# Performance work log

Measured on AMD Instinct MI355X. Metric: run time of the kernel, lower is better.

## Reference

```python
import jax, jax.numpy as jnp
import numpy as np

MODEL_DIM = 1024
ATTEN_DIM = 64
HEAD_NUM = 16
EPS = 1e-5


def setup_inputs() -> dict:
    key = jax.random.key(0)
    ks = jax.random.split(key, 10)
    B, S, D = 4, 2048, MODEL_DIM
    H = ATTEN_DIM * HEAD_NUM
    s = 1.0 / np.sqrt(D)
    return {
        "Q": jax.random.normal(ks[0], (B, S, D), dtype=jnp.float32),
        "Wq": jax.random.normal(ks[1], (D, H), dtype=jnp.float32) * s,
        "bq": jnp.zeros((H,), dtype=jnp.float32),
        "Wk": jax.random.normal(ks[2], (D, H), dtype=jnp.float32) * s,
        "bk": jnp.zeros((H,), dtype=jnp.float32),
        "Wv": jax.random.normal(ks[3], (D, H), dtype=jnp.float32) * s,
        "bv": jnp.zeros((H,), dtype=jnp.float32),
        "Wo": jax.random.normal(ks[4], (H, D), dtype=jnp.float32) * s,
        "bo": jnp.zeros((D,), dtype=jnp.float32),
        "ln_g": jnp.ones((D,), dtype=jnp.float32),
        "ln_b": jnp.zeros((D,), dtype=jnp.float32),
    }


def _layernorm(x, g, b):
    mu = jnp.mean(x, axis=-1, keepdims=True)
    var = jnp.var(x, axis=-1, keepdims=True)
    return (x - mu) * jax.lax.rsqrt(var + EPS) * g + b


def reference(Q, Wq, bq, Wk, bk, Wv, bv, Wo, bo, ln_g, ln_b):
    B, S, D = Q.shape
    residual = Q
    # projections -> [B, H, S, d]
    q = (Q @ Wq + bq).reshape(B, S, HEAD_NUM, ATTEN_DIM).transpose(0, 2, 1, 3)
    k = (Q @ Wk + bk).reshape(B, S, HEAD_NUM, ATTEN_DIM).transpose(0, 2, 1, 3)
    v = (Q @ Wv + bv).reshape(B, S, HEAD_NUM, ATTEN_DIM).transpose(0, 2, 1, 3)
    scores = jnp.einsum("bhqd,bhkd->bhqk", q, k) / np.sqrt(ATTEN_DIM).astype(np.float32)
    attn = jax.nn.softmax(scores, axis=-1)
    context = jnp.einsum("bhqk,bhkd->bhqd", attn, v)
    context = context.transpose(0, 2, 1, 3).reshape(B, S, HEAD_NUM * ATTEN_DIM)
    output = context @ Wo + bo  # dropout p=0.0 -> identity
    return _layernorm(output + residual, ln_g, ln_b)
```

## Files before the change

### kernel.cpp

```cpp
#include <hip/hip_runtime.h>
#include <math.h>

#define BATCH 4
#define SEQ 2048
#define DMODEL 1024
#define NHEAD 16
#define DHEAD 64
#define MTOT (BATCH * SEQ)
#define LN_EPS 1e-5f

typedef float f4 __attribute__((ext_vector_type(4)));
typedef float f32x4 __attribute__((ext_vector_type(4)));
typedef __bf16 bf16_t;
typedef __bf16 bf16x8 __attribute__((ext_vector_type(8)));
typedef __bf16 bf16x4 __attribute__((ext_vector_type(4)));

__device__ __forceinline__ void gload_lds16(const bf16_t* g, bf16_t* l) {
    __builtin_amdgcn_global_load_lds(
        (const __attribute__((address_space(1))) void*)g,
        (__attribute__((address_space(3))) void*)l, 16, 0, 0);
}

__global__ __launch_bounds__(256) void cvt_bf16(
    const float* __restrict__ x, bf16_t* __restrict__ y, int n4)
{
    for (int i = blockIdx.x * 256 + threadIdx.x; i < n4; i += gridDim.x * 256) {
        f4 v = *(const f4*)&x[(size_t)i * 4];
        bf16x4 o;
        o[0] = (bf16_t)v[0]; o[1] = (bf16_t)v[1];
        o[2] = (bf16_t)v[2]; o[3] = (bf16_t)v[3];
        *(bf16x4*)&y[(size_t)i * 4] = o;
    }
}

__global__ __launch_bounds__(256) void wtrans4(
    const float* __restrict__ W0, const float* __restrict__ W1,
    const float* __restrict__ W2, const float* __restrict__ W3,
    bf16_t* __restrict__ Wt)
{
    __shared__ float tile[32][33];
    const int z = blockIdx.z;
    const float* W = (z == 0) ? W0 : (z == 1) ? W1 : (z == 2) ? W2 : W3;
    bf16_t* dst = Wt + (size_t)z * DMODEL * DMODEL;
    const int n0 = blockIdx.x * 32, k0 = blockIdx.y * 32;
    const int c = threadIdx.x & 31, rr = threadIdx.x >> 5;
#pragma unroll
    for (int i = 0; i < 32; i += 8)
        tile[rr + i][c] = W[(size_t)(k0 + rr + i) * DMODEL + n0 + c];
    __syncthreads();
#pragma unroll
    for (int i = 0; i < 32; i += 8)
        dst[(size_t)(n0 + rr + i) * DMODEL + k0 + c] = (bf16_t)tile[c][rr + i];
}

template<int OUT_BF16, int FUSED3>
__global__ __launch_bounds__(256) void gemm_mfma(
    const bf16_t* __restrict__ A, const bf16_t* __restrict__ Bt,
    const float* __restrict__ bias0, const float* __restrict__ bias1,
    const float* __restrict__ bias2, void* __restrict__ Cout)
{
    __shared__ bf16_t As[2][4096];
    __shared__ bf16_t Bs[2][4096];
    const int t = threadIdx.x;
    const int w = t >> 6, lane = t & 63;
    const int r16 = lane & 15, g = lane >> 4;

    const int flat = blockIdx.x;
    const int xc = flat & 7;
    const int t2 = flat >> 3;
    int nx, my;
    if (FUSED3) { nx = t2 % 24; my = 8 * xc + t2 / 24; }
    else        { nx = t2 & 7;  my = 8 * xc + (t2 >> 3); }
    const int m0 = my * 128, n0 = nx * 128;
    const int wr = w >> 1, wc = w & 1;

    const int y0 = w * 1024 + lane * 16;
    const int y1 = y0 + 4096;
    const int row0 = y0 >> 6, row1 = y1 >> 6;
    const int sl0 = ((y0 >> 4) & 3) ^ ((row0 >> 1) & 3);
    const int sl1 = ((y1 >> 4) & 3) ^ ((row1 >> 1) & 3);
    const bf16_t* a0 = A + (size_t)(m0 + row0) * DMODEL + sl0 * 8;
    const bf16_t* a1 = A + (size_t)(m0 + row1) * DMODEL + sl1 * 8;
    const bf16_t* b0 = Bt + (size_t)(n0 + row0) * DMODEL + sl0 * 8;
    const bf16_t* b1 = Bt + (size_t)(n0 + row1) * DMODEL + sl1 * 8;

    int aoff[4], boff[4];
#pragma unroll
    for (int i = 0; i < 4; ++i) {
        int ar = wr * 64 + i * 16 + r16;
        int al = ar * 64 + g * 16;
        al ^= ((ar >> 1) & 3) << 4;
        aoff[i] = al >> 1;
        int br = wc * 64 + i * 16 + r16;
        int bl = br * 64 + g * 16;
        bl ^= ((br >> 1) & 3) << 4;
        boff[i] = bl >> 1;
    }

    const int sel   = FUSED3 ? (n0 >> 10) : 0;
    const int c1b   = FUSED3 ? (n0 & 1023) : n0;
    const float* bp = (!FUSED3 || sel == 0) ? bias0 : (sel == 1) ? bias1 : bias2;
    float bvj[4];
#pragma unroll
    for (int j = 0; j < 4; ++j)
        bvj[j] = bp[c1b + wc * 64 + j * 16 + r16];

    const f32x4 z4 = {0.f, 0.f, 0.f, 0.f};
    f32x4 acc[4][4];
#pragma unroll
    for (int i = 0; i < 4; ++i)
#pragma unroll
        for (int j = 0; j < 4; ++j) acc[i][j] = z4;

#define STAGE(buf, kk) do { \
        gload_lds16(a0 + (kk), &As[buf][w * 512]); \
        gload_lds16(a1 + (kk), &As[buf][2048 + w * 512]); \
        gload_lds16(b0 + (kk), &Bs[buf][w * 512]); \
        gload_lds16(b1 + (kk), &Bs[buf][2048 + w * 512]); \
    } while (0)

    STAGE(0, 0);
    const int NKT = DMODEL / 32;
    for (int kt = 0; kt < NKT; ++kt) {
        const int cur = kt & 1;
        if (kt + 1 < NKT) {
            STAGE(cur ^ 1, (kt + 1) * 32);
            asm volatile("s_waitcnt vmcnt(4)" ::: "memory");
        } else {
            asm volatile("s_waitcnt vmcnt(0)" ::: "memory");
        }
        __builtin_amdgcn_s_barrier();

        bf16x8 af[4], bfr[4];
#pragma unroll
        for (int i = 0; i < 4; ++i) af[i] = *(const bf16x8*)&As[cur][aoff[i]];
#pragma unroll
        for (int j = 0; j < 4; ++j) bfr[j] = *(const bf16x8*)&Bs[cur][boff[j]];
#pragma unroll
        for (int i = 0; i < 4; ++i)
#pragma unroll
            for (int j = 0; j < 4; ++j)
                acc[i][j] = __builtin_amdgcn_mfma_f32_16x16x32_bf16(
                    af[i], bfr[j], acc[i][j], 0, 0, 0);

        asm volatile("s_waitcnt lgkmcnt(0)" ::: "memory");
        __builtin_amdgcn_s_barrier();
    }
#undef STAGE

#pragma unroll
    for (int j = 0; j < 4; ++j) {
        const int colw = (FUSED3 ? c1b : n0) + wc * 64 + j * 16 + r16;
        const float bv = bvj[j];
#pragma unroll
        for (int i = 0; i < 4; ++i) {
            const int rbase = m0 + wr * 64 + i * 16 + g * 4;
#pragma unroll
            for (int rr = 0; rr < 4; ++rr) {
                float vv = acc[i][j][rr] + bv;
                if (OUT_BF16)
                    ((bf16_t*)Cout)[(size_t)sel * (MTOT * DMODEL) +
                                    (size_t)(rbase + rr) * DMODEL + colw] = (bf16_t)vv;
                else
                    ((float*)Cout)[(size_t)(rbase + rr) * DMODEL + colw] = vv;
            }
        }
    }
}

__global__ __launch_bounds__(512) void flash_mfma(
    const bf16_t* __restrict__ qg, const bf16_t* __restrict__ kg,
    const bf16_t* __restrict__ vg, bf16_t* __restrict__ ctx)
{
    __shared__ bf16_t Ks[2][128 * 64];
    __shared__ bf16_t Vt[2][64 * 64];
    __shared__ bf16_t Ps[128 * 64];

    const int t = threadIdx.x;
    const int w = t >> 6, lane = t & 63;
    const int r16 = lane & 15, g = lane >> 4;
    const int g4 = g * 4;

    const int flat = blockIdx.x;
    const int xc  = flat & 7;
    const int kk  = flat >> 3;
    const int gid = ((kk >> 4) << 3) | xc;
    const int qt  = kk & 15;
    const int b = gid >> 4, h = gid & 15;
    const int q0 = qt * 128;

    bf16x8 qf0, qf1;
    {
        const bf16_t* qrow = qg + (size_t)(b * SEQ + q0 + 16 * w + r16) * DMODEL + h * DHEAD;
        qf0 = *(const bf16x8*)&qrow[g * 8];
        qf1 = *(const bf16x8*)&qrow[32 + g * 8];
    }

    const int yk0 = w * 1024 + lane * 16;
    const int yk1 = yk0 + 8192;
    const int kr0 = yk0 >> 7, kr1 = yk1 >> 7;
    const int ks0 = ((yk0 >> 4) & 7) ^ (kr0 & 7);
    const int ks1 = ((yk1 >> 4) & 7) ^ (kr1 & 7);
    const bf16_t* kb0 = kg + (size_t)(b * SEQ + kr0) * DMODEL + h * DHEAD + ks0 * 8;
    const bf16_t* kb1 = kg + (size_t)(b * SEQ + kr1) * DMODEL + h * DHEAD + ks1 * 8;
    const int kdo0 = w * 512, kdo1 = 4096 + w * 512;

    const bf16_t* vb0 = vg + (size_t)(b * SEQ + lane) * DMODEL + h * DHEAD + w * 8;
    const bf16_t* vb1 = vb0 + (size_t)64 * DMODEL;

    const int klin0 = ((r16 * 128 + g * 16) ^ ((r16 & 7) << 4)) >> 1;
    const int klin1 = ((r16 * 128 + 64 + g * 16) ^ ((r16 & 7) << 4)) >> 1;

    const int lu = lane >> 3, l7 = lane & 7;
    const int qs = r16 & 7;

    const f32x4 z4 = {0.f, 0.f, 0.f, 0.f};
    float l2 = 0.f;
    f32x4 o_[4];
#pragma unroll
    for (int i = 0; i < 4; ++i) o_[i] = z4;

    const float C2 = 0.1803368801f;
    const float M2 = 17.31234049f;

    gload_lds16(kb0, &Ks[0][kdo0]);
    gload_lds16(kb1, &Ks[0][kdo1]);
    bf16x8 vcur0 = *(const bf16x8*)vb0;
    bf16x8 vcur1 = *(const bf16x8*)vb1;
    bf16x8 vnxt0 = vcur0, vnxt1 = vcur1;

    const int NT = SEQ / 128;
    for (int it = 0; it < NT; ++it) {
        const int cur = it & 1;
        const int kv0 = it * 128;

#pragma unroll
        for (int e = 0; e < 8; ++e) {
            const int dst = (w * 8 + e) * 64 + (((lu ^ e) << 3) | l7);
            Vt[0][dst] = vcur0[e];
            Vt[1][dst] = vcur1[e];
        }

        asm volatile("s_waitcnt lgkmcnt(0)" ::: "memory");
        __builtin_amdgcn_s_barrier();

        if (it + 1 < NT) {
            gload_lds16(kb0 + (size_t)(kv0 + 128) * DMODEL, &Ks[cur ^ 1][kdo0]);
            gload_lds16(kb1 + (size_t)(kv0 + 128) * DMODEL, &Ks[cur ^ 1][kdo1]);
            vnxt0 = *(const bf16x8*)(vb0 + (size_t)(kv0 + 128) * DMODEL);
            vnxt1 = *(const bf16x8*)(vb1 + (size_t)(kv0 + 128) * DMODEL);
        }

        f32x4 s[8];
        __builtin_amdgcn_s_setprio(1);
#pragma unroll
        for (int nj = 0; nj < 8; ++nj) {
            bf16x8 kf0 = *(const bf16x8*)&Ks[cur][klin0 + nj * 1024];
            bf16x8 kf1 = *(const bf16x8*)&Ks[cur][klin1 + nj * 1024];
            s[nj] = __builtin_amdgcn_mfma_f32_16x16x32_bf16(kf0, qf0, z4, 0, 0, 0);
            s[nj] = __builtin_amdgcn_mfma_f32_16x16x32_bf16(kf1, qf1, s[nj], 0, 0, 0);
        }
        __builtin_amdgcn_s_setprio(0);

#pragma unroll
        for (int half = 0; half < 2; ++half) {
            const int nb = half * 4;

            float p[4][4];
            float rs = 0.f;
#pragma unroll
            for (int j = 0; j < 4; ++j)
#pragma unroll
                for (int rr = 0; rr < 4; ++rr) {
                    p[j][rr] = __builtin_amdgcn_exp2f(s[nb + j][rr] * C2 - M2);
                    rs += p[j][rr];
                }
            l2 += rs;

            const int qrow = 16 * w + r16;
#pragma unroll
            for (int j = 0; j < 4; ++j) {
                bf16x4 pk;
                pk[0] = (bf16_t)p[j][0]; pk[1] = (bf16_t)p[j][1];
                pk[2] = (bf16_t)p[j][2]; pk[3] = (bf16_t)p[j][3];
                *(bf16x4*)&Ps[qrow * 64 +
                    ((((2 * j + (g >> 1)) ^ qs) << 3) | ((g & 1) << 2))] = pk;
            }
            asm volatile("s_waitcnt lgkmcnt(0)" ::: "memory");
            bf16x8 pf0 = *(const bf16x8*)&Ps[qrow * 64 + ((g ^ qs) << 3)];
            bf16x8 pf1 = *(const bf16x8*)&Ps[qrow * 64 + (((4 + g) ^ qs) << 3)];

            __builtin_amdgcn_s_setprio(1);
#pragma unroll
            for (int dj = 0; dj < 4; ++dj) {
                const int d = dj * 16 + r16;
                bf16x8 vf0 = *(const bf16x8*)&Vt[half][d * 64 + ((g ^ qs) << 3)];
                bf16x8 vf1 = *(const bf16x8*)&Vt[half][d * 64 + (((4 + g) ^ qs) << 3)];
                o_[dj] = __builtin_amdgcn_mfma_f32_16x16x32_bf16(pf0, vf0, o_[dj], 0, 0, 0);
                o_[dj] = __builtin_amdgcn_mfma_f32_16x16x32_bf16(pf1, vf1, o_[dj], 0, 0, 0);
            }
            __builtin_amdgcn_s_setprio(0);
        }

        asm volatile("s_waitcnt lgkmcnt(0)" ::: "memory");
        __builtin_amdgcn_s_barrier();

        vcur0 = vnxt0; vcur1 = vnxt1;
    }

    l2 += __shfl_xor(l2, 16);
    l2 += __shfl_xor(l2, 32);

#pragma unroll
    for (int rr = 0; rr < 4; ++rr) {
        const float lv = __shfl(l2, g4 + rr, 16);
        const float inv = 1.0f / lv;
        const size_t rowbase =
            (size_t)(b * SEQ + q0 + 16 * w + g4 + rr) * DMODEL + h * DHEAD;
#pragma unroll
        for (int dj = 0; dj < 4; ++dj)
            ctx[rowbase + dj * 16 + r16] = (bf16_t)(o_[dj][rr] * inv);
    }
}

__global__ __launch_bounds__(256) void ln_residual(
    const bf16_t* __restrict__ x, const float* __restrict__ res,
    const float* __restrict__ g, const float* __restrict__ bb,
    float* __restrict__ out)
{
    const int row = blockIdx.x;
    const int t = threadIdx.x;
    bf16x4 xv = *(const bf16x4*)&x[(size_t)row * DMODEL + t * 4];
    f4 rv = *(const f4*)&res[(size_t)row * DMODEL + t * 4];
    f4 v;
#pragma unroll
    for (int u = 0; u < 4; ++u) v[u] = (float)xv[u] + rv[u];

    float s = 0.f, s2 = 0.f;
#pragma unroll
    for (int u = 0; u < 4; ++u) { s += v[u]; s2 += v[u] * v[u]; }
#pragma unroll
    for (int off = 1; off < 64; off <<= 1) {
        s  += __shfl_xor(s, off);
        s2 += __shfl_xor(s2, off);
    }
    __shared__ float red[2][4];
    const int wid = t >> 6, lane = t & 63;
    if (lane == 0) { red[0][wid] = s; red[1][wid] = s2; }
    __syncthreads();
    s  = red[0][0] + red[0][1] + red[0][2] + red[0][3];
    s2 = red[1][0] + red[1][1] + red[1][2] + red[1][3];

    const float mean = s * (1.0f / DMODEL);
    const float var  = s2 * (1.0f / DMODEL) - mean * mean;
    const float rstd = rsqrtf(var + LN_EPS);

    f4 gv = *(const f4*)&g[t * 4];
    f4 bv = *(const f4*)&bb[t * 4];
    f4 ov;
#pragma unroll
    for (int u = 0; u < 4; ++u) ov[u] = (v[u] - mean) * rstd * gv[u] + bv[u];
    *(f4*)&out[(size_t)row * DMODEL + t * 4] = ov;
}

extern "C" void kernel_launch(void* const* d_in, const int* in_sizes, int n_in,
                              void* d_out, int out_size, void* d_ws, size_t ws_size,
                              hipStream_t stream)
{
    const float* Q   = (const float*)d_in[0];
    const float* Wq  = (const float*)d_in[1];
    const float* bq  = (const float*)d_in[2];
    const float* Wk  = (const float*)d_in[3];
    const float* bk  = (const float*)d_in[4];
    const float* Wv  = (const float*)d_in[5];
    const float* bv  = (const float*)d_in[6];
    const float* Wo  = (const float*)d_in[7];
    const float* bo  = (const float*)d_in[8];
    const float* lng = (const float*)d_in[9];
    const float* lnb = (const float*)d_in[10];

    char* wsb = (char*)d_ws;
    bf16_t* Qbf  = (bf16_t*)(wsb);
    bf16_t* qb   = (bf16_t*)(wsb + (size_t)(16 << 20));
    bf16_t* kb   = (bf16_t*)(wsb + (size_t)(32 << 20));
    bf16_t* vbuf = (bf16_t*)(wsb + (size_t)(48 << 20));
    bf16_t* aob  = (bf16_t*)(wsb + (size_t)(32 << 20));
    bf16_t* Wqt  = (bf16_t*)(wsb + (size_t)(64 << 20));
    bf16_t* Wot  = (bf16_t*)(wsb + (size_t)(70 << 20));

    cvt_bf16<<<2048, 256, 0, stream>>>(Q, Qbf, MTOT * DMODEL / 4);
    wtrans4<<<dim3(32, 32, 4), 256, 0, stream>>>(Wq, Wk, Wv, Wo, Wqt);

    gemm_mfma<1, 1><<<24 * 64, 256, 0, stream>>>(Qbf, Wqt, bq, bk, bv, qb);

    const int agrid = (SEQ / 128) * NHEAD * BATCH;
    flash_mfma<<<agrid, 512, 0, stream>>>(qb, kb, vbuf, qb);

    gemm_mfma<1, 0><<<8 * 64, 256, 0, stream>>>(qb, Wot, bo, bo, bo, aob);

    ln_residual<<<MTOT, 256, 0, stream>>>(aob, Q, lng, lnb, (float*)d_out);
}
```

Measured before the change: 234.7 us.

## Process two 16-row query tiles per wave in flash attention with 256 threads

The attention kernel now uses 4 waves instead of 8, and each wave handles 32 query rows as two 16-row tiles. Each K and V fragment read from LDS is therefore reused for two MFMA streams. Each thread loads twice as much K and V data per iteration. This cuts LDS read traffic and barrier participants per unit of work, at the cost of more registers per wave and fewer waves per block for hiding latency.

Result: no change. 235.3 us (+0.3%).

```diff
diff --git a/kernel.cpp b/kernel.cpp
--- a/kernel.cpp
+++ b/kernel.cpp
@@ -168,7 +168,7 @@
     }
 }
 
-__global__ __launch_bounds__(512) void flash_mfma(
+__global__ __launch_bounds__(256, 2) void flash_mfma(
     const bf16_t* __restrict__ qg, const bf16_t* __restrict__ kg,
     const bf16_t* __restrict__ vg, bf16_t* __restrict__ ctx)
 {
@@ -189,23 +189,28 @@
     const int b = gid >> 4, h = gid & 15;
     const int q0 = qt * 128;
 
-    bf16x8 qf0, qf1;
+    bf16x8 qfA0, qfA1, qfB0, qfB1;
     {
-        const bf16_t* qrow = qg + (size_t)(b * SEQ + q0 + 16 * w + r16) * DMODEL + h * DHEAD;
-        qf0 = *(const bf16x8*)&qrow[g * 8];
-        qf1 = *(const bf16x8*)&qrow[32 + g * 8];
-    }
-
-    const int yk0 = w * 1024 + lane * 16;
-    const int yk1 = yk0 + 8192;
-    const int kr0 = yk0 >> 7, kr1 = yk1 >> 7;
-    const int ks0 = ((yk0 >> 4) & 7) ^ (kr0 & 7);
-    const int ks1 = ((yk1 >> 4) & 7) ^ (kr1 & 7);
-    const bf16_t* kb0 = kg + (size_t)(b * SEQ + kr0) * DMODEL + h * DHEAD + ks0 * 8;
-    const bf16_t* kb1 = kg + (size_t)(b * SEQ + kr1) * DMODEL + h * DHEAD + ks1 * 8;
-    const int kdo0 = w * 512, kdo1 = 4096 + w * 512;
-
-    const bf16_t* vb0 = vg + (size_t)(b * SEQ + lane) * DMODEL + h * DHEAD + w * 8;
+        const bf16_t* qrA = qg + (size_t)(b * SEQ + q0 + 32 * w + r16) * DMODEL + h * DHEAD;
+        const bf16_t* qrB = qrA + (size_t)16 * DMODEL;
+        qfA0 = *(const bf16x8*)&qrA[g * 8];
+        qfA1 = *(const bf16x8*)&qrA[32 + g * 8];
+        qfB0 = *(const bf16x8*)&qrB[g * 8];
+        qfB1 = *(const bf16x8*)&qrB[32 + g * 8];
+    }
+
+    const bf16_t* kb[4];
+    int kdo[4];
+#pragma unroll
+    for (int r = 0; r < 4; ++r) {
+        const int y = r * 4096 + w * 1024 + lane * 16;
+        const int krow = y >> 7;
+        const int kslot = ((y >> 4) & 7) ^ (krow & 7);
+        kb[r] = kg + (size_t)(b * SEQ + krow) * DMODEL + h * DHEAD + kslot * 8;
+        kdo[r] = r * 2048 + w * 512;
+    }
+
+    const bf16_t* vb0 = vg + (size_t)(b * SEQ + lane) * DMODEL + h * DHEAD + w * 16;
     const bf16_t* vb1 = vb0 + (size_t)64 * DMODEL;
 
     const int klin0 = ((r16 * 128 + g * 16) ^ ((r16 & 7) << 4)) >> 1;
@@ -215,19 +220,21 @@
     const int qs = r16 & 7;
 
     const f32x4 z4 = {0.f, 0.f, 0.f, 0.f};
-    float l2 = 0.f;
-    f32x4 o_[4];
-#pragma unroll
-    for (int i = 0; i < 4; ++i) o_[i] = z4;
+    float l2A = 0.f, l2B = 0.f;
+    f32x4 oA[4], oB[4];
+#pragma unroll
+    for (int i = 0; i < 4; ++i) { oA[i] = z4; oB[i] = z4; }
 
     const float C2 = 0.1803368801f;
     const float M2 = 17.31234049f;
 
-    gload_lds16(kb0, &Ks[0][kdo0]);
-    gload_lds16(kb1, &Ks[0][kdo1]);
-    bf16x8 vcur0 = *(const bf16x8*)vb0;
-    bf16x8 vcur1 = *(const bf16x8*)vb1;
-    bf16x8 vnxt0 = vcur0, vnxt1 = vcur1;
+#pragma unroll
+    for (int r = 0; r < 4; ++r) gload_lds16(kb[r], &Ks[0][kdo[r]]);
+    bf16x8 vc0a = *(const bf16x8*)&vb0[0];
+    bf16x8 vc0b = *(const bf16x8*)&vb0[8];
+    bf16x8 vc1a = *(const bf16x8*)&vb1[0];
+    bf16x8 vc1b = *(const bf16x8*)&vb1[8];
+    bf16x8 vn0a = vc0a, vn0b = vc0b, vn1a = vc1a, vn1b = vc1b;
 
     const int NT = SEQ / 128;
     for (int it = 0; it < NT; ++it) {
@@ -236,59 +243,78 @@
 
 #pragma unroll
         for (int e = 0; e < 8; ++e) {
-            const int dst = (w * 8 + e) * 64 + (((lu ^ e) << 3) | l7);
-            Vt[0][dst] = vcur0[e];
-            Vt[1][dst] = vcur1[e];
+            const int dst0 = (w * 16 + e) * 64 + (((lu ^ e) << 3) | l7);
+            const int dst1 = (w * 16 + 8 + e) * 64 + (((lu ^ e) << 3) | l7);
+            Vt[0][dst0] = vc0a[e];
+            Vt[1][dst0] = vc1a[e];
+            Vt[0][dst1] = vc0b[e];
+            Vt[1][dst1] = vc1b[e];
         }
 
         asm volatile("s_waitcnt lgkmcnt(0)" ::: "memory");
         __builtin_amdgcn_s_barrier();
 
         if (it + 1 < NT) {
-            gload_lds16(kb0 + (size_t)(kv0 + 128) * DMODEL, &Ks[cur ^ 1][kdo0]);
-            gload_lds16(kb1 + (size_t)(kv0 + 128) * DMODEL, &Ks[cur ^ 1][kdo1]);
-            vnxt0 = *(const bf16x8*)(vb0 + (size_t)(kv0 + 128) * DMODEL);
-            vnxt1 = *(const bf16x8*)(vb1 + (size_t)(kv0 + 128) * DMODEL);
-        }
-
-        f32x4 s[8];
+#pragma unroll
+            for (int r = 0; r < 4; ++r)
+                gload_lds16(kb[r] + (size_t)(kv0 + 128) * DMODEL, &Ks[cur ^ 1][kdo[r]]);
+            const bf16_t* v0 = vb0 + (size_t)(kv0 + 128) * DMODEL;
+            const bf16_t* v1 = vb1 + (size_t)(kv0 + 128) * DMODEL;
+            vn0a = *(const bf16x8*)&v0[0];
+            vn0b = *(const bf16x8*)&v0[8];
+            vn1a = *(const bf16x8*)&v1[0];
+            vn1b = *(const bf16x8*)&v1[8];
+        }
+
+        f32x4 sA[8], sB[8];
         __builtin_amdgcn_s_setprio(1);
 #pragma unroll
         for (int nj = 0; nj < 8; ++nj) {
             bf16x8 kf0 = *(const bf16x8*)&Ks[cur][klin0 + nj * 1024];
             bf16x8 kf1 = *(const bf16x8*)&Ks[cur][klin1 + nj * 1024];
-            s[nj] = __builtin_amdgcn_mfma_f32_16x16x32_bf16(kf0, qf0, z4, 0, 0, 0);
-            s[nj] = __builtin_amdgcn_mfma_f32_16x16x32_bf16(kf1, qf1, s[nj], 0, 0, 0);
+            sA[nj] = __builtin_amdgcn_mfma_f32_16x16x32_bf16(kf0, qfA0, z4, 0, 0, 0);
+            sA[nj] = __builtin_amdgcn_mfma_f32_16x16x32_bf16(kf1, qfA1, sA[nj], 0, 0, 0);
+            sB[nj] = __builtin_amdgcn_mfma_f32_16x16x32_bf16(kf0, qfB0, z4, 0, 0, 0);
+            sB[nj] = __builtin_amdgcn_mfma_f32_16x16x32_bf16(kf1, qfB1, sB[nj], 0, 0, 0);
         }
         __builtin_amdgcn_s_setprio(0);
 
 #pragma unroll
         for (int half = 0; half < 2; ++half) {
             const int nb = half * 4;
-
-            float p[4][4];
-            float rs = 0.f;
+            const int qrA = 32 * w + r16;
+            const int qrB = qrA + 16;
+
+            float pA[4][4], pB[4][4];
+            float rsA = 0.f, rsB = 0.f;
 #pragma unroll
             for (int j = 0; j < 4; ++j)
 #pragma unroll
                 for (int rr = 0; rr < 4; ++rr) {
-                    p[j][rr] = __builtin_amdgcn_exp2f(s[nb + j][rr] * C2 - M2);
-                    rs += p[j][rr];
+                    pA[j][rr] = __builtin_amdgcn_exp2f(sA[nb + j][rr] * C2 - M2);
+                    rsA += pA[j][rr];
+                    pB[j][rr] = __builtin_amdgcn_exp2f(sB[nb + j][rr] * C2 - M2);
+                    rsB += pB[j][rr];
                 }
-            l2 += rs;
-
-            const int qrow = 16 * w + r16;
+            l2A += rsA;
+            l2B += rsB;
+
 #pragma unroll
             for (int j = 0; j < 4; ++j) {
-                bf16x4 pk;
-                pk[0] = (bf16_t)p[j][0]; pk[1] = (bf16_t)p[j][1];
-                pk[2] = (bf16_t)p[j][2]; pk[3] = (bf16_t)p[j][3];
-                *(bf16x4*)&Ps[qrow * 64 +
-                    ((((2 * j + (g >> 1)) ^ qs) << 3) | ((g & 1) << 2))] = pk;
+                bf16x4 pkA, pkB;
+                pkA[0] = (bf16_t)pA[j][0]; pkA[1] = (bf16_t)pA[j][1];
+                pkA[2] = (bf16_t)pA[j][2]; pkA[3] = (bf16_t)pA[j][3];
+                pkB[0] = (bf16_t)pB[j][0]; pkB[1] = (bf16_t)pB[j][1];
+                pkB[2] = (bf16_t)pB[j][2]; pkB[3] = (bf16_t)pB[j][3];
+                const int u = ((((2 * j + (g >> 1)) ^ qs) << 3) | ((g & 1) << 2));
+                *(bf16x4*)&Ps[qrA * 64 + u] = pkA;
+                *(bf16x4*)&Ps[qrB * 64 + u] = pkB;
             }
             asm volatile("s_waitcnt lgkmcnt(0)" ::: "memory");
-            bf16x8 pf0 = *(const bf16x8*)&Ps[qrow * 64 + ((g ^ qs) << 3)];
-            bf16x8 pf1 = *(const bf16x8*)&Ps[qrow * 64 + (((4 + g) ^ qs) << 3)];
+            bf16x8 pfA0 = *(const bf16x8*)&Ps[qrA * 64 + ((g ^ qs) << 3)];
+            bf16x8 pfA1 = *(const bf16x8*)&Ps[qrA * 64 + (((4 + g) ^ qs) << 3)];
+            bf16x8 pfB0 = *(const bf16x8*)&Ps[qrB * 64 + ((g ^ qs) << 3)];
+            bf16x8 pfB1 = *(const bf16x8*)&Ps[qrB * 64 + (((4 + g) ^ qs) << 3)];
 
             __builtin_amdgcn_s_setprio(1);
 #pragma unroll
@@ -296,8 +322,10 @@
                 const int d = dj * 16 + r16;
                 bf16x8 vf0 = *(const bf16x8*)&Vt[half][d * 64 + ((g ^ qs) << 3)];
                 bf16x8 vf1 = *(const bf16x8*)&Vt[half][d * 64 + (((4 + g) ^ qs) << 3)];
-                o_[dj] = __builtin_amdgcn_mfma_f32_16x16x32_bf16(pf0, vf0, o_[dj], 0, 0, 0);
-                o_[dj] = __builtin_amdgcn_mfma_f32_16x16x32_bf16(pf1, vf1, o_[dj], 0, 0, 0);
+                oA[dj] = __builtin_amdgcn_mfma_f32_16x16x32_bf16(pfA0, vf0, oA[dj], 0, 0, 0);
+                oA[dj] = __builtin_amdgcn_mfma_f32_16x16x32_bf16(pfA1, vf1, oA[dj], 0, 0, 0);
+                oB[dj] = __builtin_amdgcn_mfma_f32_16x16x32_bf16(pfB0, vf0, oB[dj], 0, 0, 0);
+                oB[dj] = __builtin_amdgcn_mfma_f32_16x16x32_bf16(pfB1, vf1, oB[dj], 0, 0, 0);
             }
             __builtin_amdgcn_s_setprio(0);
         }
@@ -305,21 +333,26 @@
         asm volatile("s_waitcnt lgkmcnt(0)" ::: "memory");
         __builtin_amdgcn_s_barrier();
 
-        vcur0 = vnxt0; vcur1 = vnxt1;
-    }
-
-    l2 += __shfl_xor(l2, 16);
-    l2 += __shfl_xor(l2, 32);
+        vc0a = vn0a; vc0b = vn0b; vc1a = vn1a; vc1b = vn1b;
+    }
+
+    l2A += __shfl_xor(l2A, 16);
+    l2A += __shfl_xor(l2A, 32);
+    l2B += __shfl_xor(l2B, 16);
+    l2B += __shfl_xor(l2B, 32);
 
 #pragma unroll
     for (int rr = 0; rr < 4; ++rr) {
-        const float lv = __shfl(l2, g4 + rr, 16);
-        const float inv = 1.0f / lv;
-        const size_t rowbase =
-            (size_t)(b * SEQ + q0 + 16 * w + g4 + rr) * DMODEL + h * DHEAD;
-#pragma unroll
-        for (int dj = 0; dj < 4; ++dj)
-            ctx[rowbase + dj * 16 + r16] = (bf16_t)(o_[dj][rr] * inv);
+        const float invA = 1.0f / __shfl(l2A, g4 + rr, 16);
+        const float invB = 1.0f / __shfl(l2B, g4 + rr, 16);
+        const size_t rbA =
+            (size_t)(b * SEQ + q0 + 32 * w + g4 + rr) * DMODEL + h * DHEAD;
+        const size_t rbB = rbA + (size_t)16 * DMODEL;
+#pragma unroll
+        for (int dj = 0; dj < 4; ++dj) {
+            ctx[rbA + dj * 16 + r16] = (bf16_t)(oA[dj][rr] * invA);
+            ctx[rbB + dj * 16 + r16] = (bf16_t)(oB[dj][rr] * invB);
+        }
     }
 }
 
@@ -394,7 +427,7 @@
     gemm_mfma<1, 1><<<24 * 64, 256, 0, stream>>>(Qbf, Wqt, bq, bk, bv, qb);
 
     const int agrid = (SEQ / 128) * NHEAD * BATCH;
-    flash_mfma<<<agrid, 512, 0, stream>>>(qb, kb, vbuf, qb);
+    flash_mfma<<<agrid, 256, 0, stream>>>(qb, kb, vbuf, qb);
 
     gemm_mfma<1, 0><<<8 * 64, 256, 0, stream>>>(qb, Wot, bo, bo, bo, aob);
 
```
